# Optimization experiments

Hardware: AMD Instinct MI355X
Metric: run time of the kernel (lower is better)

Reference implementation:

```python
import jax, jax.numpy as jnp
import numpy as np

C = 16       # channel_n
WDIM = 64    # w_dim
HID = 128    # hidden_n
B, H, W = 16, 128, 128


def setup_inputs() -> dict:
    key = jax.random.key(0)
    k_x, k_w, k_w1, k_w2 = jax.random.split(key, 4)
    x = jax.random.normal(k_x, (B, C, H, W), dtype=jnp.float32)
    w = jax.random.normal(k_w, (B, WDIM), dtype=jnp.float32)
    # update_net: Linear(3C+WDIM -> HID), ReLU, Linear(HID -> C)  (torch layout: [out, in])
    W1 = jax.random.normal(k_w1, (HID, 3 * C + WDIM), dtype=jnp.float32) * 0.05
    b1 = jnp.zeros((HID,), dtype=jnp.float32)
    W2 = jax.random.normal(k_w2, (C, HID), dtype=jnp.float32) * 0.05
    b2 = jnp.zeros((C,), dtype=jnp.float32)
    sx = jnp.array([[-1, 0, 1], [-2, 0, 2], [-1, 0, 1]], dtype=jnp.float32)
    sy = jnp.array([[-1, -2, -1], [0, 0, 0], [1, 2, 1]], dtype=jnp.float32)
    sobel_x = jnp.tile(sx[None, None], (C, 1, 1, 1))  # [C,1,3,3] depthwise kernel
    sobel_y = jnp.tile(sy[None, None], (C, 1, 1, 1))
    return {"x": x, "w": w, "W1": W1, "b1": b1, "W2": W2, "b2": b2,
            "sobel_x": sobel_x, "sobel_y": sobel_y, "steps": 10}


def _dwconv(x, k):
    # depthwise 3x3 conv, SAME padding, groups = channel_n
    return jax.lax.conv_general_dilated(
        x, k, window_strides=(1, 1), padding='SAME',
        feature_group_count=x.shape[1],
        dimension_numbers=('NCHW', 'OIHW', 'NCHW'))


def _maxpool3(a):
    # 3x3 max pool, stride 1, SAME padding on [B,1,H,W]
    return jax.lax.reduce_window(a, -jnp.inf, jax.lax.max,
                                 (1, 1, 3, 3), (1, 1, 1, 1), 'SAME')


def reference(x, w, W1, b1, W2, b2, sobel_x, sobel_y, steps):
    b, c, h, ww = x.shape
    wdim = w.shape[1]
    w_bcast = jnp.broadcast_to(w[:, None, None, :], (b, h, ww, wdim))
    for _ in range(steps):
        pre_life = (_maxpool3(x[:, 3:4]) > 0.1).astype(x.dtype)  # [B,1,H,W]
        gx = _dwconv(x, sobel_x)
        gy = _dwconv(x, sobel_y)
        perceived = jnp.concatenate([x, gx, gy], axis=1)            # [B,3C,H,W]
        perceived = jnp.transpose(perceived, (0, 2, 3, 1))          # [B,H,W,3C]
        inp = jnp.concatenate([perceived, w_bcast], axis=-1)        # [B,H,W,3C+WDIM]
        hdd = jax.nn.relu(jnp.einsum('bhwc,nc->bhwn', inp, W1) + b1)
        ds = jnp.einsum('bhwn,cn->bhwc', hdd, W2) + b2              # [B,H,W,C]
        x = x + jnp.transpose(ds, (0, 3, 1, 2))
        life = (x[:, 3:4] > 0.1).astype(x.dtype) * pre_life
        x = x * life
    return x
```

## Files before the change

### kernel.cpp

```cpp
#include <hip/hip_runtime.h>


#define CCH   16
#define WDIM  64
#define HID   128
#define BATCH 16
#define HH    128
#define WWID  128
#define KIN   48
#define NIN   112
#define TS    16
#define HALO  18
#define STEPS 10

__global__ __launch_bounds__(256) void nca_prep_kernel(
    const float* __restrict__ W1, const float* __restrict__ b1,
    const float* __restrict__ w,  const float* __restrict__ W2,
    float* __restrict__ biasw, float* __restrict__ W1t, float* __restrict__ W2t)
{
    const int t = threadIdx.x;
    for (int i = t; i < KIN * HID; i += 256) {
        int k = i / HID, n = i % HID;
        W1t[k * HID + n] = W1[n * NIN + k];
    }
    for (int i = t; i < HID * CCH; i += 256) {
        int n = i / CCH, c = i % CCH;
        W2t[n * CCH + c] = W2[c * HID + n];
    }
    for (int i = t; i < BATCH * HID; i += 256) {
        int b = i / HID, n = i % HID;
        float acc = b1[n];
        const float* wrow  = w  + b * WDIM;
        const float* W1row = W1 + n * NIN + KIN;
        #pragma unroll
        for (int j = 0; j < WDIM; ++j) acc = fmaf(W1row[j], wrow[j], acc);
        biasw[i] = acc;
    }
}

__global__ __launch_bounds__(256, 2) void nca_step_kernel(
    const float* __restrict__ xin, float* __restrict__ xout,
    const float* __restrict__ W1t, const float* __restrict__ W2t,
    const float* __restrict__ b2, const float* __restrict__ biasw)
{
    __shared__ float tile[CCH][HALO][HALO];

    const int b   = blockIdx.z;
    const int ty0 = blockIdx.y * TS;
    const int tx0 = blockIdx.x * TS;
    const int tid = threadIdx.x;

    const float* xb = xin + b * CCH * HH * WWID;
    for (int idx = tid; idx < CCH * HALO * HALO; idx += 256) {
        int c  = idx / (HALO * HALO);
        int r  = idx % (HALO * HALO);
        int ly = r / HALO, lx = r % HALO;
        int gy = ty0 + ly - 1, gx = tx0 + lx - 1;
        float v = 0.f;
        if (gy >= 0 && gy < HH && gx >= 0 && gx < WWID)
            v = xb[c * HH * WWID + gy * WWID + gx];
        tile[c][ly][lx] = v;
    }
    __syncthreads();

    const int ty = tid >> 4, tx = tid & 15;
    const int ly = ty + 1,  lx = tx + 1;

    float inp[KIN];
    bool pre_life = false;
    #pragma unroll
    for (int c = 0; c < CCH; ++c) {
        float x_mm = tile[c][ly-1][lx-1], x_m0 = tile[c][ly-1][lx], x_mp = tile[c][ly-1][lx+1];
        float x_0m = tile[c][ly  ][lx-1], x_00 = tile[c][ly  ][lx], x_0p = tile[c][ly  ][lx+1];
        float x_pm = tile[c][ly+1][lx-1], x_p0 = tile[c][ly+1][lx], x_pp = tile[c][ly+1][lx+1];
        inp[c] = x_00;
        inp[CCH   + c] = (x_mp - x_mm) + 2.f * (x_0p - x_0m) + (x_pp - x_pm);
        inp[2*CCH + c] = (x_pm - x_mm) + 2.f * (x_p0 - x_m0) + (x_pp - x_mp);
        if (c == 3) {
            float m = fmaxf(fmaxf(fmaxf(x_mm, x_m0), fmaxf(x_mp, x_0m)),
                            fmaxf(fmaxf(x_00, x_0p), fmaxf(x_pm, fmaxf(x_p0, x_pp))));
            pre_life = (m > 0.1f);
        }
    }

    float ds[CCH];
    #pragma unroll
    for (int c = 0; c < CCH; ++c) ds[c] = b2[c];

    const float* biasb = biasw + b * HID;
    #pragma unroll 1
    for (int h0 = 0; h0 < HID; h0 += 16) {
        float hh[16];
        #pragma unroll
        for (int n = 0; n < 16; ++n) hh[n] = biasb[h0 + n];
        #pragma unroll
        for (int k = 0; k < KIN; ++k) {
            float iv = inp[k];
            const float* wrow = W1t + k * HID + h0;
            #pragma unroll
            for (int n = 0; n < 16; ++n)
                hh[n] = fmaf(iv, wrow[n], hh[n]);
        }
        #pragma unroll
        for (int n = 0; n < 16; ++n) hh[n] = fmaxf(hh[n], 0.f);
        #pragma unroll
        for (int n = 0; n < 16; ++n) {
            float hv = hh[n];
            const float* w2row = W2t + (h0 + n) * CCH;
            #pragma unroll
            for (int c = 0; c < CCH; ++c)
                ds[c] = fmaf(hv, w2row[c], ds[c]);
        }
    }

    float new3  = inp[3] + ds[3];
    float alive = ((new3 > 0.1f) && pre_life) ? 1.f : 0.f;
    float* ob = xout + b * CCH * HH * WWID;
    const int gy = ty0 + ty, gx = tx0 + tx;
    #pragma unroll
    for (int c = 0; c < CCH; ++c) {
        float nv = inp[c] + ds[c];
        ob[c * HH * WWID + gy * WWID + gx] = nv * alive;
    }
}

extern "C" void kernel_launch(void* const* d_in, const int* in_sizes, int n_in,
                              void* d_out, int out_size, void* d_ws, size_t ws_size,
                              hipStream_t stream) {
    const float* x   = (const float*)d_in[0];
    const float* w   = (const float*)d_in[1];
    const float* W1  = (const float*)d_in[2];
    const float* b1  = (const float*)d_in[3];
    const float* W2  = (const float*)d_in[4];
    const float* b2  = (const float*)d_in[5];
    float* out = (float*)d_out;

    float* ws0   = (float*)d_ws;
    float* biasw = ws0 + BATCH * CCH * HH * WWID;
    float* W1t   = biasw + BATCH * HID;
    float* W2t   = W1t + KIN * HID;

    nca_prep_kernel<<<1, 256, 0, stream>>>(W1, b1, w, W2, biasw, W1t, W2t);

    dim3 grid(WWID / TS, HH / TS, BATCH);
    for (int s = 0; s < STEPS; ++s) {
        float* dst = (((STEPS - 1 - s) & 1) == 0) ? out : ws0;
        const float* src = (s == 0) ? x
                         : ((((STEPS - s) & 1) == 0) ? (const float*)out : (const float*)ws0);
        nca_step_kernel<<<grid, 256, 0, stream>>>(src, dst, W1t, W2t, b2, biasw);
    }
}
```

Baseline: 781.9 us.

## Restructure MLP loop to keep full hidden vector in registers per channel

Reorders the first-layer GEMV so each thread holds all 128 hidden accumulators in registers and streams channels, computing Sobel values on the fly instead of storing a 48-wide input array. W1 is repacked channel-major and interleaved (x, gx, gy) so weights are read contiguously. The residual reads x from shared memory instead of registers. This cuts live input registers and merges the per-block loop, at the cost of 128 live accumulators, which may raise register pressure or cause spills under the 2-blocks-per-SM launch bound.

```diff
diff --git a/kernel.cpp b/kernel.cpp
--- a/kernel.cpp
+++ b/kernel.cpp
@@ -16,12 +16,13 @@
 __global__ __launch_bounds__(256) void nca_prep_kernel(
     const float* __restrict__ W1, const float* __restrict__ b1,
     const float* __restrict__ w,  const float* __restrict__ W2,
-    float* __restrict__ biasw, float* __restrict__ W1t, float* __restrict__ W2t)
+    float* __restrict__ biasw, float* __restrict__ W1p, float* __restrict__ W2t)
 {
     const int t = threadIdx.x;
     for (int i = t; i < KIN * HID; i += 256) {
-        int k = i / HID, n = i % HID;
-        W1t[k * HID + n] = W1[n * NIN + k];
+        int cj = i / HID, n = i % HID;
+        int c = cj / 3, j = cj % 3;
+        W1p[i] = W1[n * NIN + j * CCH + c];
     }
     for (int i = t; i < HID * CCH; i += 256) {
         int n = i / CCH, c = i % CCH;
@@ -40,7 +41,7 @@
 
 __global__ __launch_bounds__(256, 2) void nca_step_kernel(
     const float* __restrict__ xin, float* __restrict__ xout,
-    const float* __restrict__ W1t, const float* __restrict__ W2t,
+    const float* __restrict__ W1p, const float* __restrict__ W2t,
     const float* __restrict__ b2, const float* __restrict__ biasw)
 {
     __shared__ float tile[CCH][HALO][HALO];
@@ -66,60 +67,56 @@
     const int ty = tid >> 4, tx = tid & 15;
     const int ly = ty + 1,  lx = tx + 1;
 
-    float inp[KIN];
-    bool pre_life = false;
+    bool pre_life;
+    {
+        float a0 = tile[3][ly-1][lx-1], a1 = tile[3][ly-1][lx], a2 = tile[3][ly-1][lx+1];
+        float a3 = tile[3][ly  ][lx-1], a4 = tile[3][ly  ][lx], a5 = tile[3][ly  ][lx+1];
+        float a6 = tile[3][ly+1][lx-1], a7 = tile[3][ly+1][lx], a8 = tile[3][ly+1][lx+1];
+        float m = fmaxf(fmaxf(fmaxf(a0, a1), fmaxf(a2, a3)),
+                        fmaxf(fmaxf(a4, a5), fmaxf(a6, fmaxf(a7, a8))));
+        pre_life = (m > 0.1f);
+    }
+
+    float hh[HID];
+    const float* biasb = biasw + b * HID;
     #pragma unroll
+    for (int n = 0; n < HID; ++n) hh[n] = biasb[n];
+
+    #pragma unroll 1
     for (int c = 0; c < CCH; ++c) {
         float x_mm = tile[c][ly-1][lx-1], x_m0 = tile[c][ly-1][lx], x_mp = tile[c][ly-1][lx+1];
         float x_0m = tile[c][ly  ][lx-1], x_00 = tile[c][ly  ][lx], x_0p = tile[c][ly  ][lx+1];
         float x_pm = tile[c][ly+1][lx-1], x_p0 = tile[c][ly+1][lx], x_pp = tile[c][ly+1][lx+1];
-        inp[c] = x_00;
-        inp[CCH   + c] = (x_mp - x_mm) + 2.f * (x_0p - x_0m) + (x_pp - x_pm);
-        inp[2*CCH + c] = (x_pm - x_mm) + 2.f * (x_p0 - x_m0) + (x_pp - x_mp);
-        if (c == 3) {
-            float m = fmaxf(fmaxf(fmaxf(x_mm, x_m0), fmaxf(x_mp, x_0m)),
-                            fmaxf(fmaxf(x_00, x_0p), fmaxf(x_pm, fmaxf(x_p0, x_pp))));
-            pre_life = (m > 0.1f);
+        float gxv = (x_mp - x_mm) + 2.f * (x_0p - x_0m) + (x_pp - x_pm);
+        float gyv = (x_pm - x_mm) + 2.f * (x_p0 - x_m0) + (x_pp - x_mp);
+        const float* wp = W1p + c * (3 * HID);
+        #pragma unroll
+        for (int n = 0; n < HID; ++n) {
+            float t0 = fmaf(x_00, wp[n],           hh[n]);
+            float t1 = fmaf(gxv,  wp[HID + n],     t0);
+            hh[n]    = fmaf(gyv,  wp[2 * HID + n], t1);
         }
     }
 
     float ds[CCH];
     #pragma unroll
     for (int c = 0; c < CCH; ++c) ds[c] = b2[c];
-
-    const float* biasb = biasw + b * HID;
-    #pragma unroll 1
-    for (int h0 = 0; h0 < HID; h0 += 16) {
-        float hh[16];
+    #pragma unroll
+    for (int n = 0; n < HID; ++n) {
+        float hv = fmaxf(hh[n], 0.f);
+        const float* w2row = W2t + n * CCH;
         #pragma unroll
-        for (int n = 0; n < 16; ++n) hh[n] = biasb[h0 + n];
-        #pragma unroll
-        for (int k = 0; k < KIN; ++k) {
-            float iv = inp[k];
-            const float* wrow = W1t + k * HID + h0;
-            #pragma unroll
-            for (int n = 0; n < 16; ++n)
-                hh[n] = fmaf(iv, wrow[n], hh[n]);
-        }
-        #pragma unroll
-        for (int n = 0; n < 16; ++n) hh[n] = fmaxf(hh[n], 0.f);
-        #pragma unroll
-        for (int n = 0; n < 16; ++n) {
-            float hv = hh[n];
-            const float* w2row = W2t + (h0 + n) * CCH;
-            #pragma unroll
-            for (int c = 0; c < CCH; ++c)
-                ds[c] = fmaf(hv, w2row[c], ds[c]);
-        }
+        for (int c = 0; c < CCH; ++c)
+            ds[c] = fmaf(hv, w2row[c], ds[c]);
     }
 
-    float new3  = inp[3] + ds[3];
+    float new3  = tile[3][ly][lx] + ds[3];
     float alive = ((new3 > 0.1f) && pre_life) ? 1.f : 0.f;
     float* ob = xout + b * CCH * HH * WWID;
     const int gy = ty0 + ty, gx = tx0 + tx;
     #pragma unroll
     for (int c = 0; c < CCH; ++c) {
-        float nv = inp[c] + ds[c];
+        float nv = tile[c][ly][lx] + ds[c];
         ob[c * HH * WWID + gy * WWID + gx] = nv * alive;
     }
 }
@@ -137,16 +134,16 @@
 
     float* ws0   = (float*)d_ws;
     float* biasw = ws0 + BATCH * CCH * HH * WWID;
-    float* W1t   = biasw + BATCH * HID;
-    float* W2t   = W1t + KIN * HID;
+    float* W1p   = biasw + BATCH * HID;
+    float* W2t   = W1p + KIN * HID;
 
-    nca_prep_kernel<<<1, 256, 0, stream>>>(W1, b1, w, W2, biasw, W1t, W2t);
+    nca_prep_kernel<<<1, 256, 0, stream>>>(W1, b1, w, W2, biasw, W1p, W2t);
 
     dim3 grid(WWID / TS, HH / TS, BATCH);
     for (int s = 0; s < STEPS; ++s) {
         float* dst = (((STEPS - 1 - s) & 1) == 0) ? out : ws0;
         const float* src = (s == 0) ? x
                          : ((((STEPS - s) & 1) == 0) ? (const float*)out : (const float*)ws0);
-        nca_step_kernel<<<grid, 256, 0, stream>>>(src, dst, W1t, W2t, b2, biasw);
+        nca_step_kernel<<<grid, 256, 0, stream>>>(src, dst, W1p, W2t, b2, biasw);
     }
 }
```

Result: slower. 1.227 ms (+57.0%).
